# Kernel optimization log

Hardware: AMD Instinct MI355X
Metric: run time of the kernel (lower is better)

The kernel has to match this reference:

```python
import jax, jax.numpy as jnp
import numpy as np

DIM = 256
N_EMBED = 8192
DECAY = 0.1
COMMITMENT = 1.0
EPS = 1e-05


def setup_inputs() -> dict:
    key = jax.random.key(0)
    k1, k2, k3, k4 = jax.random.split(key, 4)
    return {
        "input": jax.random.normal(k1, (8, 1024, DIM), dtype=jnp.float32),
        "embed": jax.random.normal(k2, (DIM, N_EMBED), dtype=jnp.float32),
        "cluster_size": jax.random.uniform(k3, (N_EMBED,), dtype=jnp.float32),
        "embed_avg": jax.random.normal(k4, (DIM, N_EMBED), dtype=jnp.float32),
    }


def reference(input, embed, cluster_size, embed_avg):
    dtype = input.dtype
    flatten = input.reshape(-1, DIM)  # [N, dim]
    # squared euclidean distance to each code: [N, n_embed]
    dist = (
        jnp.sum(flatten * flatten, axis=1, keepdims=True)
        - 2.0 * (flatten @ embed)
        + jnp.sum(embed * embed, axis=0, keepdims=True)
    )
    embed_ind_flat = jnp.argmin(dist, axis=1)  # [N]
    embed_ind = embed_ind_flat.reshape(input.shape[:-1])
    quantize = jnp.take(embed.T, embed_ind, axis=0)  # [..., dim]

    # EMA codebook update (training path), via segment sums instead of dense one-hot
    bins = jax.ops.segment_sum(
        jnp.ones_like(embed_ind_flat, dtype=dtype), embed_ind_flat, num_segments=N_EMBED
    )  # one_hot.sum(0)
    embed_sum = jax.ops.segment_sum(flatten, embed_ind_flat, num_segments=N_EMBED).T  # [dim, n_embed]
    cluster_size_new = cluster_size * DECAY + (1.0 - DECAY) * bins
    embed_avg_new = embed_avg * DECAY + (1.0 - DECAY) * embed_sum
    smoothed = (cluster_size_new + EPS) / (jnp.sum(cluster_size_new) + N_EMBED * EPS)
    cs = smoothed * jnp.sum(cluster_size_new)
    embed_normalized = embed_avg_new / cs[None, :]

    commit_loss = jnp.mean((jax.lax.stop_gradient(quantize) - input) ** 2) * COMMITMENT
    quantize_st = input + jax.lax.stop_gradient(quantize - input)
    return (quantize_st, embed_ind, commit_loss, embed_normalized, cluster_size_new, embed_avg_new)
```

## Files before the change

### kernel.cpp

```cpp
#include <hip/hip_runtime.h>

typedef unsigned short u16;
typedef __attribute__((ext_vector_type(8))) short short8;
typedef __attribute__((ext_vector_type(4))) float f32x4;

#define DIM    256
#define NE     8192
#define NROWS  8192
#define DECAY  0.1f
#define EPS_F  1e-5f
#define CRANGES 16
#define CPAIRS  16
#define MQ      384u

#define OUT_Q    0
#define OUT_IND  2097152
#define OUT_LOSS 2105344
#define OUT_NORM 2105345
#define OUT_CSN  4202497
#define OUT_AVG  4210689

#define WS_CAND  65536
#define WS_ENORM 1114112
#define WS_BASEQ 1146880
#define WS_SUM   1179648
#define WS_BINS  9568256
#define WS_LOSS  9601024
#define WS_SCS   9601032
#define WS_XB    9601040
#define WS_ETB   13795344
#define WS_ET32  17989648
#define ZERO_F4  ((WS_LOSS - WS_SUM) / 16)

__device__ __forceinline__ unsigned f32_ord(float f)
{
    unsigned u = __float_as_uint(f);
    return (u & 0x80000000u) ? ~u : (u | 0x80000000u);
}
__device__ __forceinline__ u16 bf16rne(float f)
{
    unsigned u = __float_as_uint(f);
    return (u16)((u + 0x7fffu + ((u >> 16) & 1u)) >> 16);
}
__device__ __forceinline__ void gload16(const void* g, void* l)
{
    __builtin_amdgcn_global_load_lds((const __attribute__((address_space(1))) unsigned int*)g,
                                     (__attribute__((address_space(3))) unsigned int*)l, 16, 0, 0);
}

__global__ __launch_bounds__(256) void vq_prep_k(const float* __restrict__ X,
                                                 const float* __restrict__ E,
                                                 const float* __restrict__ CS,
                                                 u16* __restrict__ Xb,
                                                 float* __restrict__ ET32,
                                                 u16* __restrict__ ETb,
                                                 float* __restrict__ enorm,
                                                 float* __restrict__ baseq,
                                                 double* __restrict__ sumcs,
                                                 double* __restrict__ loss,
                                                 char* __restrict__ ws)
{
    const int bid = blockIdx.x;
    const int t = threadIdx.x;

    if (bid < 128) {
        __shared__ float T[64][65];
        const int j0 = bid * 64;
        const int jc = t >> 2, seg = t & 3;
        const int j = j0 + jc;
        float esum = 0.f;
        for (int d0 = 0; d0 < DIM; d0 += 64) {
            if (d0) __syncthreads();
            #pragma unroll
            for (int p = 0; p < 4; ++p) {
                const int dr = p * 16 + (t >> 4);
                const float4 v = *(const float4*)(E + (size_t)(d0 + dr) * NE + j0 + (t & 15) * 4);
                T[dr][(t & 15) * 4 + 0] = v.x; T[dr][(t & 15) * 4 + 1] = v.y;
                T[dr][(t & 15) * 4 + 2] = v.z; T[dr][(t & 15) * 4 + 3] = v.w;
            }
            __syncthreads();
            float vals[16];
            #pragma unroll
            for (int i = 0; i < 16; ++i) vals[i] = T[seg * 16 + i][jc];
            float4* o32 = (float4*)(ET32 + (size_t)j * DIM + d0 + seg * 16);
            o32[0] = make_float4(vals[0], vals[1], vals[2], vals[3]);
            o32[1] = make_float4(vals[4], vals[5], vals[6], vals[7]);
            o32[2] = make_float4(vals[8], vals[9], vals[10], vals[11]);
            o32[3] = make_float4(vals[12], vals[13], vals[14], vals[15]);
            short8 b0, b1;
            #pragma unroll
            for (int i = 0; i < 8; ++i) { b0[i] = (short)bf16rne(vals[i]); b1[i] = (short)bf16rne(vals[8 + i]); }
            *(short8*)(ETb + (size_t)j * DIM + d0 + seg * 16) = b0;
            *(short8*)(ETb + (size_t)j * DIM + d0 + seg * 16 + 8) = b1;
            #pragma unroll
            for (int i = 0; i < 16; ++i) esum += vals[i] * vals[i];
        }
        esum += __shfl_xor(esum, 1, 4);
        esum += __shfl_xor(esum, 2, 4);
        if (seg == 0) {
            enorm[j] = esum;
            baseq[j] = (esum + 512.f) * 256.f;
        }
    } else if (bid < 256) {
        const int chunk = bid - 128;
        #pragma unroll
        for (int it = 0; it < 8; ++it) {
            const int gi = chunk * 2048 + it * 256 + t;
            const float4 a = ((const float4*)X)[gi * 2];
            const float4 b = ((const float4*)X)[gi * 2 + 1];
            short8 v;
            v[0] = (short)bf16rne(a.x); v[1] = (short)bf16rne(a.y);
            v[2] = (short)bf16rne(a.z); v[3] = (short)bf16rne(a.w);
            v[4] = (short)bf16rne(b.x); v[5] = (short)bf16rne(b.y);
            v[6] = (short)bf16rne(b.z); v[7] = (short)bf16rne(b.w);
            *(short8*)(Xb + (size_t)gi * 8) = v;
        }
    } else if (bid == 256) {
        double s = 0.0;
        #pragma unroll
        for (int it = 0; it < 8; ++it) {
            const float4 v = ((const float4*)CS)[it * 256 + t];
            s += (double)v.x + (double)v.y + (double)v.z + (double)v.w;
        }
        #pragma unroll
        for (int off = 32; off > 0; off >>= 1) s += __shfl_down(s, off);
        __shared__ double wred[4];
        if ((t & 63) == 0) wred[t >> 6] = s;
        __syncthreads();
        if (t == 0) {
            sumcs[0] = wred[0] + wred[1] + wred[2] + wred[3];
            loss[0]  = 0.0;
        }
    } else {
        float4* z = (float4*)(ws + WS_SUM);
        const float4 zv = make_float4(0.f, 0.f, 0.f, 0.f);
        for (int i = (bid - 257) * 256 + t; i < ZERO_F4; i += 128 * 256) z[i] = zv;
    }
}

__global__ __launch_bounds__(256, 2) void vq_scan_k(const u16* __restrict__ Xb,
                                                    const u16* __restrict__ ETb,
                                                    const float* __restrict__ baseq,
                                                    unsigned* __restrict__ cand)
{
    __shared__ u16 Bs[2][16][512];
    __shared__ float Bq[512];

    const int tid = threadIdx.x;
    const int w = tid >> 6, l = tid & 63;
    const int lane16 = l & 15, g = l >> 4;
    const int rowbase = blockIdx.x * 256 + w * 64;
    const int c0 = blockIdx.y * 512;

    const float2 bq2 = *(const float2*)(baseq + c0 + tid * 2);

    short8 af[4][8];
    #pragma unroll
    for (int sub = 0; sub < 4; ++sub)
        #pragma unroll
        for (int k8 = 0; k8 < 8; ++k8) {
            af[sub][k8] = *(const short8*)(Xb + (size_t)(rowbase + sub * 16 + lane16) * DIM + k8 * 32 + g * 8);
            asm volatile("" : "+a"(af[sub][k8]));
        }

    *(float2*)&Bq[tid * 2] = bq2;

    unsigned s0[16], s1[16];
    #pragma unroll
    for (int i = 0; i < 16; ++i) { s0[i] = 0xFFFFFFFFu; s1[i] = 0xFFFFFFFFu; }

    const u16* gsrc = ETb + (size_t)(c0 + lane16) * DIM + (size_t)w * 64 + g * 8;

    gload16(gsrc,                 &Bs[0][2 * w + 0][0]);
    gload16(gsrc + 32,            &Bs[0][2 * w + 1][0]);
    gload16(gsrc + 16 * DIM,      &Bs[0][8 + 2 * w + 0][0]);
    gload16(gsrc + 16 * DIM + 32, &Bs[0][8 + 2 * w + 1][0]);
    asm volatile("s_waitcnt lgkmcnt(0)" ::: "memory");
    __builtin_amdgcn_s_barrier();

    int buf = 0;
    #pragma unroll 1
    for (int p = 0; p < CPAIRS; ++p) {
        if (p + 1 < CPAIRS) {
            const u16* nsrc = gsrc + (size_t)(p + 1) * 32 * DIM;
            gload16(nsrc,                 &Bs[buf ^ 1][2 * w + 0][0]);
            gload16(nsrc + 32,            &Bs[buf ^ 1][2 * w + 1][0]);
            gload16(nsrc + 16 * DIM,      &Bs[buf ^ 1][8 + 2 * w + 0][0]);
            gload16(nsrc + 16 * DIM + 32, &Bs[buf ^ 1][8 + 2 * w + 1][0]);
            asm volatile("s_waitcnt vmcnt(4)" ::: "memory");
        } else {
            asm volatile("s_waitcnt vmcnt(0)" ::: "memory");
        }
        __builtin_amdgcn_s_barrier();

        #pragma unroll
        for (int half = 0; half < 2; ++half) {
            const int ct = p * 2 + half;
            const int col = c0 + ct * 16 + lane16;
            const float bq = Bq[ct * 16 + lane16];
            f32x4 acc[4];
            #pragma unroll
            for (int sub = 0; sub < 4; ++sub) acc[sub] = {0.f, 0.f, 0.f, 0.f};
            #pragma unroll
            for (int k8 = 0; k8 < 8; ++k8) {
                const short8 bf = *(const short8*)&Bs[buf][half * 8 + k8][l * 8];
                #pragma unroll
                for (int sub = 0; sub < 4; ++sub)
                    acc[sub] = __builtin_amdgcn_mfma_f32_16x16x32_bf16(af[sub][k8], bf, acc[sub], 0, 0, 0);
            }
            #pragma unroll
            for (int sub = 0; sub < 4; ++sub)
                #pragma unroll
                for (int r = 0; r < 4; ++r) {
                    const int i = sub * 4 + r;
                    const float qf = fmaf(acc[sub][r], -512.f, bq);
                    const unsigned key = (((unsigned)qf) << 13) | (unsigned)col;
                    const unsigned tt = max(s0[i], key);
                    s0[i] = min(s0[i], key);
                    s1[i] = min(s1[i], tt);
                }
        }
        __builtin_amdgcn_s_barrier();
        buf ^= 1;
    }

    #pragma unroll
    for (int m = 1; m < 16; m <<= 1) {
        #pragma unroll
        for (int i = 0; i < 16; ++i) {
            const unsigned o0 = __shfl_xor(s0[i], m);
            const unsigned o1 = __shfl_xor(s1[i], m);
            const unsigned t0 = min(s0[i], o0);
            const unsigned t1 = min(max(s0[i], o0), min(s1[i], o1));
            s0[i] = t0; s1[i] = t1;
        }
    }
    if (lane16 == 0) {
        #pragma unroll
        for (int i = 0; i < 16; ++i) {
            const int row = rowbase + (i >> 2) * 16 + g * 4 + (i & 3);
            cand[((size_t)row * CRANGES + blockIdx.y) * 2 + 0] = s0[i];
            cand[((size_t)row * CRANGES + blockIdx.y) * 2 + 1] = s1[i];
        }
    }
}

__global__ __launch_bounds__(256) void vq_finalize_k(const unsigned* __restrict__ cand,
                                                     const float* __restrict__ X,
                                                     const float* __restrict__ ET32,
                                                     const float* __restrict__ enorm,
                                                     float* __restrict__ out_q,
                                                     float* __restrict__ out_ind,
                                                     float* __restrict__ ws_sum,
                                                     float* __restrict__ bins,
                                                     double* __restrict__ loss)
{
    __shared__ int sj[4];
    const int tid = threadIdx.x;
    const int w = tid >> 6, l = tid & 63;
    const int row = blockIdx.x * 4 + w;

    unsigned key = 0xFFFFFFFFu;
    if (l < 32) key = cand[(size_t)row * 32 + l];
    unsigned qmin = key;
    #pragma unroll
    for (int m = 32; m; m >>= 1) qmin = min(qmin, __shfl_xor(qmin, m));
    const unsigned qthr = (qmin >> 13) + MQ;
    unsigned long long mask = __ballot((l < 32) && ((key >> 13) <= qthr));
    const float4 xv = *(const float4*)(X + (size_t)row * DIM + l * 4);
    unsigned long long best = 0xFFFFFFFFFFFFFFFFull;
    while (mask) {
        const int src = __builtin_ctzll(mask);
        mask &= mask - 1;
        const int col = (int)(__shfl(key, src) & 8191u);
        const float4 ev = *(const float4*)(ET32 + (size_t)col * DIM + l * 4);
        float s = xv.x * ev.x + xv.y * ev.y + xv.z * ev.z + xv.w * ev.w;
        #pragma unroll
        for (int m = 32; m; m >>= 1) s += __shfl_xor(s, m);
        const float d = enorm[col] - 2.f * s;
        const unsigned long long k64 = ((unsigned long long)f32_ord(d) << 32) | (unsigned)col;
        best = (k64 < best) ? k64 : best;
    }
    if (l == 0) {
        const int j = (int)(best & 8191u);
        sj[w] = j;
        out_ind[row] = (float)j;
    }
    __syncthreads();

    float lsum = 0.f;
    #pragma unroll
    for (int q = 0; q < 4; ++q) {
        const int r = blockIdx.x * 4 + q;
        const int j = sj[q];
        const float x  = X[(size_t)r * DIM + tid];
        const float qv = ET32[(size_t)j * DIM + tid];
        out_q[(size_t)r * DIM + tid] = x + (qv - x);
        const float d = qv - x;
        lsum += d * d;
        atomicAdd(&ws_sum[(size_t)j * DIM + tid], x);
        if (tid == 0) atomicAdd(&bins[j], 1.0f);
    }
    #pragma unroll
    for (int off = 32; off > 0; off >>= 1) lsum += __shfl_down(lsum, off);
    __shared__ double wred[4];
    if ((tid & 63) == 0) wred[tid >> 6] = (double)lsum;
    __syncthreads();
    if (tid == 0) atomicAdd(loss, wred[0] + wred[1] + wred[2] + wred[3]);
}

__global__ __launch_bounds__(256) void vq_embed_k(const float* __restrict__ EA,
                                                  const float* __restrict__ cs,
                                                  const float* __restrict__ bins,
                                                  const float* __restrict__ ws_sum,
                                                  const double* __restrict__ sumcs,
                                                  const double* __restrict__ loss,
                                                  float* __restrict__ out_norm,
                                                  float* __restrict__ out_avg,
                                                  float* __restrict__ out_csn,
                                                  float* __restrict__ out_loss)
{
    __shared__ float T[64][69];
    const int tid = threadIdx.x;
    const int j0 = blockIdx.x * 64;
    const int d0 = blockIdx.y * 64;
    #pragma unroll
    for (int p = 0; p < 4; ++p) {
        const int jr = (tid >> 4) + p * 16;
        const int dc = (tid & 15) * 4;
        const float4 v = *(const float4*)(ws_sum + (size_t)(j0 + jr) * DIM + d0 + dc);
        T[jr][dc + 0] = v.x; T[jr][dc + 1] = v.y; T[jr][dc + 2] = v.z; T[jr][dc + 3] = v.w;
    }
    __syncthreads();
    const double S = (double)DECAY * sumcs[0] + (double)(1.0f - DECAY) * (double)NROWS;
    const float fac = (float)(S / (S + (double)NE * 1e-5));
    const int jc = tid & 63;
    const int j  = j0 + jc;
    const float csn  = cs[j] * DECAY + (1.0f - DECAY) * bins[j];
    const float cs_j = (csn + EPS_F) * fac;
    if (blockIdx.y == 0 && tid < 64) out_csn[j0 + tid] = cs[j0 + tid] * DECAY + (1.0f - DECAY) * bins[j0 + tid];
    if (blockIdx.y == 0 && blockIdx.x == 0 && tid == 0) out_loss[0] = (float)(loss[0] * (1.0 / 2097152.0));
    const int drb = (tid >> 6) * 16;
    #pragma unroll
    for (int p = 0; p < 16; ++p) {
        const int dr = drb + p;
        const float sum = T[jc][dr];
        const float ea  = EA[(size_t)(d0 + dr) * NE + j];
        const float ean = DECAY * ea + (1.0f - DECAY) * sum;
        out_avg[(size_t)(d0 + dr) * NE + j]  = ean;
        out_norm[(size_t)(d0 + dr) * NE + j] = ean / cs_j;
    }
}

extern "C" void kernel_launch(void* const* d_in, const int* in_sizes, int n_in,
                              void* d_out, int out_size, void* d_ws, size_t ws_size,
                              hipStream_t stream)
{
    const float* X  = (const float*)d_in[0];
    const float* E  = (const float*)d_in[1];
    const float* CS = (const float*)d_in[2];
    const float* EA = (const float*)d_in[3];
    float* out = (float*)d_out;
    char*  ws  = (char*)d_ws;

    unsigned* cand  = (unsigned*)(ws + WS_CAND);
    float*  enorm  = (float*)(ws + WS_ENORM);
    float*  baseq  = (float*)(ws + WS_BASEQ);
    float*  ws_sum = (float*)(ws + WS_SUM);
    float*  bins   = (float*)(ws + WS_BINS);
    double* loss   = (double*)(ws + WS_LOSS);
    double* sumcs  = (double*)(ws + WS_SCS);
    u16*    Xb     = (u16*)(ws + WS_XB);
    u16*    ETb    = (u16*)(ws + WS_ETB);
    float*  ET32   = (float*)(ws + WS_ET32);

    vq_prep_k<<<385, 256, 0, stream>>>(X, E, CS, Xb, ET32, ETb, enorm, baseq, sumcs, loss, ws);
    vq_scan_k<<<dim3(NROWS / 256, CRANGES), 256, 0, stream>>>(Xb, ETb, baseq, cand);
    vq_finalize_k<<<NROWS / 4, 256, 0, stream>>>(cand, X, ET32, enorm, out + OUT_Q, out + OUT_IND, ws_sum, bins, loss);
    vq_embed_k<<<dim3(NE / 64, DIM / 64), 256, 0, stream>>>(EA, CS, bins, ws_sum, sumcs, loss,
                                                            out + OUT_NORM, out + OUT_AVG, out + OUT_CSN, out + OUT_LOSS);
}
```

Measured before the change: 100.9 us.

## Give each wave private LDS codebook tiles to remove block barriers in scan loop

The scan kernel no longer shares one double-buffered codebook tile across all four waves. Each wave now loads its own full 16-column tile into a per-wave double-buffered LDS slot and prefetches two tiles ahead. This removes the two workgroup barriers per iteration, letting waves run independently. In exchange each wave loads the whole tile redundantly, which quadruples global/L2 traffic for codebook data and LDS use (64KB), possibly lowering occupancy.

```diff
diff --git a/kernel.cpp b/kernel.cpp
--- a/kernel.cpp
+++ b/kernel.cpp
@@ -10,7 +10,7 @@
 #define DECAY  0.1f
 #define EPS_F  1e-5f
 #define CRANGES 16
-#define CPAIRS  16
+#define CTILES  32
 #define MQ      384u
 
 #define OUT_Q    0
@@ -143,7 +143,7 @@
                                                     const float* __restrict__ baseq,
                                                     unsigned* __restrict__ cand)
 {
-    __shared__ u16 Bs[2][16][512];
+    __shared__ u16 Bs[4][2][8][512];
     __shared__ float Bq[512];
 
     const int tid = threadIdx.x;
@@ -152,7 +152,7 @@
     const int rowbase = blockIdx.x * 256 + w * 64;
     const int c0 = blockIdx.y * 512;
 
-    const float2 bq2 = *(const float2*)(baseq + c0 + tid * 2);
+    *(float2*)&Bq[tid * 2] = *(const float2*)(baseq + c0 + tid * 2);
 
     short8 af[4][8];
     #pragma unroll
@@ -163,65 +163,56 @@
             asm volatile("" : "+a"(af[sub][k8]));
         }
 
-    *(float2*)&Bq[tid * 2] = bq2;
+    __syncthreads();
 
     unsigned s0[16], s1[16];
     #pragma unroll
     for (int i = 0; i < 16; ++i) { s0[i] = 0xFFFFFFFFu; s1[i] = 0xFFFFFFFFu; }
 
-    const u16* gsrc = ETb + (size_t)(c0 + lane16) * DIM + (size_t)w * 64 + g * 8;
-
-    gload16(gsrc,                 &Bs[0][2 * w + 0][0]);
-    gload16(gsrc + 32,            &Bs[0][2 * w + 1][0]);
-    gload16(gsrc + 16 * DIM,      &Bs[0][8 + 2 * w + 0][0]);
-    gload16(gsrc + 16 * DIM + 32, &Bs[0][8 + 2 * w + 1][0]);
-    asm volatile("s_waitcnt lgkmcnt(0)" ::: "memory");
-    __builtin_amdgcn_s_barrier();
-
-    int buf = 0;
+    const u16* gsrc = ETb + (size_t)(c0 + lane16) * DIM + g * 8;
+
+    #pragma unroll
+    for (int s = 0; s < 8; ++s) gload16(gsrc + s * 32, &Bs[w][0][s][0]);
+    #pragma unroll
+    for (int s = 0; s < 8; ++s) gload16(gsrc + 16 * DIM + s * 32, &Bs[w][1][s][0]);
+
     #pragma unroll 1
-    for (int p = 0; p < CPAIRS; ++p) {
-        if (p + 1 < CPAIRS) {
-            const u16* nsrc = gsrc + (size_t)(p + 1) * 32 * DIM;
-            gload16(nsrc,                 &Bs[buf ^ 1][2 * w + 0][0]);
-            gload16(nsrc + 32,            &Bs[buf ^ 1][2 * w + 1][0]);
-            gload16(nsrc + 16 * DIM,      &Bs[buf ^ 1][8 + 2 * w + 0][0]);
-            gload16(nsrc + 16 * DIM + 32, &Bs[buf ^ 1][8 + 2 * w + 1][0]);
-            asm volatile("s_waitcnt vmcnt(4)" ::: "memory");
-        } else {
-            asm volatile("s_waitcnt vmcnt(0)" ::: "memory");
-        }
-        __builtin_amdgcn_s_barrier();
-
-        #pragma unroll
-        for (int half = 0; half < 2; ++half) {
-            const int ct = p * 2 + half;
-            const int col = c0 + ct * 16 + lane16;
-            const float bq = Bq[ct * 16 + lane16];
-            f32x4 acc[4];
-            #pragma unroll
-            for (int sub = 0; sub < 4; ++sub) acc[sub] = {0.f, 0.f, 0.f, 0.f};
-            #pragma unroll
-            for (int k8 = 0; k8 < 8; ++k8) {
-                const short8 bf = *(const short8*)&Bs[buf][half * 8 + k8][l * 8];
-                #pragma unroll
-                for (int sub = 0; sub < 4; ++sub)
-                    acc[sub] = __builtin_amdgcn_mfma_f32_16x16x32_bf16(af[sub][k8], bf, acc[sub], 0, 0, 0);
+    for (int t = 0; t < CTILES; ++t) {
+        if (t < CTILES - 1) asm volatile("s_waitcnt vmcnt(8)" ::: "memory");
+        else                asm volatile("s_waitcnt vmcnt(0)" ::: "memory");
+
+        const int slot = t & 1;
+        const float bq = Bq[t * 16 + lane16];
+        f32x4 acc[4];
+        #pragma unroll
+        for (int sub = 0; sub < 4; ++sub) acc[sub] = {0.f, 0.f, 0.f, 0.f};
+        #pragma unroll
+        for (int k8 = 0; k8 < 8; ++k8) {
+            const short8 bf = *(const short8*)&Bs[w][slot][k8][l * 8];
+            #pragma unroll
+            for (int sub = 0; sub < 4; ++sub)
+                acc[sub] = __builtin_amdgcn_mfma_f32_16x16x32_bf16(af[sub][k8], bf, acc[sub], 0, 0, 0);
+        }
+
+        asm volatile("s_waitcnt lgkmcnt(0)" ::: "memory");
+        if (t + 2 < CTILES) {
+            const u16* nsrc = gsrc + (size_t)(t + 2) * 16 * DIM;
+            #pragma unroll
+            for (int s = 0; s < 8; ++s) gload16(nsrc + s * 32, &Bs[w][slot][s][0]);
+        }
+
+        const int col = c0 + t * 16 + lane16;
+        #pragma unroll
+        for (int sub = 0; sub < 4; ++sub)
+            #pragma unroll
+            for (int r = 0; r < 4; ++r) {
+                const int i = sub * 4 + r;
+                const float qf = fmaf(acc[sub][r], -512.f, bq);
+                const unsigned key = (((unsigned)qf) << 13) | (unsigned)col;
+                const unsigned tt = max(s0[i], key);
+                s0[i] = min(s0[i], key);
+                s1[i] = min(s1[i], tt);
             }
-            #pragma unroll
-            for (int sub = 0; sub < 4; ++sub)
-                #pragma unroll
-                for (int r = 0; r < 4; ++r) {
-                    const int i = sub * 4 + r;
-                    const float qf = fmaf(acc[sub][r], -512.f, bq);
-                    const unsigned key = (((unsigned)qf) << 13) | (unsigned)col;
-                    const unsigned tt = max(s0[i], key);
-                    s0[i] = min(s0[i], key);
-                    s1[i] = min(s1[i], tt);
-                }
-        }
-        __builtin_amdgcn_s_barrier();
-        buf ^= 1;
     }
 
     #pragma unroll
```

Measured after the change: 124.6 us. +23.5%, slower.
